# Optimization experiments

Hardware: AMD Instinct MI355X
Metric: run time of the kernel (lower is better)

Reference implementation:

```python
import jax, jax.numpy as jnp
import numpy as np

LN_EPS = 1e-5

def setup_inputs() -> dict:
    key = jax.random.key(0)
    ks = jax.random.split(key, 4)
    B, D, H, K = 8192, 4096, 2048, 512
    return {
        "x": jax.random.normal(ks[0], (B, D), jnp.float32),
        "beta": jax.random.normal(ks[1], (D, K), jnp.float32) * 0.01,
        "compound_mean": jnp.zeros((D,), jnp.float32),
        "W1": jax.random.normal(ks[2], (H, D), jnp.float32) * 0.02,
        "b1": jnp.zeros((H,), jnp.float32),
        "ln_w": jnp.ones((H,), jnp.float32),
        "ln_b": jnp.zeros((H,), jnp.float32),
        "W2": jax.random.normal(ks[3], (K, H), jnp.float32) * 0.02,
        "b2": jnp.zeros((K,), jnp.float32),
    }

def reference(x, beta, compound_mean, W1, b1, ln_w, ln_b, W2, b2):
    # compound path of BiQBMVAE.forward (compound=True)
    h = jnp.einsum('bd,hd->bh', x - compound_mean, W1) + b1      # fc1
    mu = jnp.mean(h, axis=-1, keepdims=True)                      # LayerNorm
    var = jnp.mean(jnp.square(h - mu), axis=-1, keepdims=True)
    h = (h - mu) * jax.lax.rsqrt(var + LN_EPS) * ln_w + ln_b
    h = jax.nn.relu(h)                                            # act_fn
    q_logits = jnp.einsum('bh,kh->bk', h, W2) + b2                # fc2 -> [B, k]
    x_recon = jax.nn.sigmoid(jnp.einsum('bk,dk->bd', q_logits, beta))  # decode_compound
    return (q_logits, x_recon, q_logits, q_logits)
```

## Files before the change

kernel.cpp:

```cpp
#include <hip/hip_runtime.h>
#include <hip/hip_bf16.h>
#include <cstddef>
#include <cstdint>

#define LN_EPS 1e-5f

#define B_DIM 8192
#define D_DIM 4096
#define H_DIM 2048
#define K_DIM 512

typedef __bf16 bf16x8_t __attribute__((ext_vector_type(8)));
typedef float f32x4_t __attribute__((ext_vector_type(4)));

__device__ __forceinline__ void gl2lds16(const __hip_bfloat16* g,
                                         __hip_bfloat16* l) {
  __builtin_amdgcn_global_load_lds(
      (const __attribute__((address_space(1))) uint32_t*)g,
      (__attribute__((address_space(3))) uint32_t*)l, 16, 0, 0);
}

__global__ __launch_bounds__(256) void conv_x_kernel(
    const float* __restrict__ x, const float* __restrict__ cmean,
    __hip_bfloat16* __restrict__ out) {
  const long i = (((long)blockIdx.x << 8) + threadIdx.x) << 3;
  const int col = (int)(i & (D_DIM - 1));
  const float4 a = *(const float4*)(x + i);
  const float4 b = *(const float4*)(x + i + 4);
  const float4 ma = *(const float4*)(cmean + col);
  const float4 mb = *(const float4*)(cmean + col + 4);
  union { __hip_bfloat16 h[8]; uint4 u; } pk;
  pk.h[0] = __float2bfloat16(a.x - ma.x);
  pk.h[1] = __float2bfloat16(a.y - ma.y);
  pk.h[2] = __float2bfloat16(a.z - ma.z);
  pk.h[3] = __float2bfloat16(a.w - ma.w);
  pk.h[4] = __float2bfloat16(b.x - mb.x);
  pk.h[5] = __float2bfloat16(b.y - mb.y);
  pk.h[6] = __float2bfloat16(b.z - mb.z);
  pk.h[7] = __float2bfloat16(b.w - mb.w);
  *(uint4*)(out + i) = pk.u;
}

__global__ __launch_bounds__(256) void conv_w3_kernel(
    const float* __restrict__ W1, const float* __restrict__ W2,
    const float* __restrict__ beta, __hip_bfloat16* __restrict__ W1b,
    __hip_bfloat16* __restrict__ W2b, __hip_bfloat16* __restrict__ betab) {
  const int blk = blockIdx.x;
  const float* src;
  __hip_bfloat16* dst;
  long base;
  if (blk < 4096) {
    src = W1; dst = W1b; base = blk;
  } else if (blk < 4608) {
    src = W2; dst = W2b; base = blk - 4096;
  } else {
    src = beta; dst = betab; base = blk - 4608;
  }
  const long i = ((base << 8) + threadIdx.x) << 3;
  const float4 a = *(const float4*)(src + i);
  const float4 b = *(const float4*)(src + i + 4);
  union { __hip_bfloat16 h[8]; uint4 u; } pk;
  pk.h[0] = __float2bfloat16(a.x);
  pk.h[1] = __float2bfloat16(a.y);
  pk.h[2] = __float2bfloat16(a.z);
  pk.h[3] = __float2bfloat16(a.w);
  pk.h[4] = __float2bfloat16(b.x);
  pk.h[5] = __float2bfloat16(b.y);
  pk.h[6] = __float2bfloat16(b.z);
  pk.h[7] = __float2bfloat16(b.w);
  *(uint4*)(dst + i) = pk.u;
}

template <int EPI>
__global__ __launch_bounds__(256) void gemm_bt(
    const __hip_bfloat16* __restrict__ A, int lda,
    const __hip_bfloat16* __restrict__ Bm, int ldb,
    const float* __restrict__ bias, float* __restrict__ C0, int ldc,
    float* __restrict__ C2, float* __restrict__ C3,
    __hip_bfloat16* __restrict__ Cb, int Kd) {
  __shared__ __hip_bfloat16 lA[128 * 32];
  __shared__ __hip_bfloat16 lB[128 * 32];

  const int t = threadIdx.x;
  const int lane = t & 63;
  const int wv = t >> 6;
  const int wm = (wv >> 1) * 64;
  const int wn = (wv & 1) * 64;
  const int fr = lane & 15;
  const int ko = lane >> 4;
  const int kos = (ko ^ ((fr >> 1) & 3)) * 8;

  const long rowA = (long)blockIdx.y * 128;
  const long rowB = (long)blockIdx.x * 128;

  const int ci = wv * 128 + lane;
  const int srow = ci >> 2;
  const int scol = (((ci & 3) ^ ((ci >> 3) & 3))) * 8;
  const __hip_bfloat16* pA0 = A + (rowA + srow) * (long)lda + scol;
  const __hip_bfloat16* pA1 = pA0 + 16L * lda;
  const __hip_bfloat16* pB0 = Bm + (rowB + srow) * (long)ldb + scol;
  const __hip_bfloat16* pB1 = pB0 + 16L * ldb;
  __hip_bfloat16* lA0 = lA + wv * 128 * 8;
  __hip_bfloat16* lA1 = lA0 + 64 * 8;
  __hip_bfloat16* lB0 = lB + wv * 128 * 8;
  __hip_bfloat16* lB1 = lB0 + 64 * 8;

  f32x4_t acc[4][4];
  const f32x4_t zero = {0.f, 0.f, 0.f, 0.f};
#pragma unroll
  for (int mi = 0; mi < 4; ++mi)
#pragma unroll
    for (int ni = 0; ni < 4; ++ni) acc[mi][ni] = zero;

  for (int k0 = 0; k0 < Kd; k0 += 32) {
    gl2lds16(pA0 + k0, lA0);
    gl2lds16(pA1 + k0, lA1);
    gl2lds16(pB0 + k0, lB0);
    gl2lds16(pB1 + k0, lB1);
    __syncthreads();

    bf16x8_t af[4], bfv[4];
#pragma unroll
    for (int mi = 0; mi < 4; ++mi)
      af[mi] = *(const bf16x8_t*)&lA[(wm + mi * 16 + fr) * 32 + kos];
#pragma unroll
    for (int ni = 0; ni < 4; ++ni)
      bfv[ni] = *(const bf16x8_t*)&lB[(wn + ni * 16 + fr) * 32 + kos];
#pragma unroll
    for (int mi = 0; mi < 4; ++mi)
#pragma unroll
      for (int ni = 0; ni < 4; ++ni)
        acc[mi][ni] = __builtin_amdgcn_mfma_f32_16x16x32_bf16(
            af[mi], bfv[ni], acc[mi][ni], 0, 0, 0);
    __syncthreads();
  }

  const long cRow0 = rowA + wm;
  const int cCol0 = (int)rowB + wn;
#pragma unroll
  for (int mi = 0; mi < 4; ++mi) {
#pragma unroll
    for (int ni = 0; ni < 4; ++ni) {
      f32x4_t a = acc[mi][ni];
      int col = cCol0 + ni * 16 + fr;
#pragma unroll
      for (int r = 0; r < 4; ++r) {
        long row = cRow0 + mi * 16 + ko * 4 + r;
        float val = a[r];
        if constexpr (EPI == 0) {
          val += bias[col];
          C0[row * (long)ldc + col] = val;
        } else if constexpr (EPI == 1) {
          val += bias[col];
          C0[row * (long)ldc + col] = val;
          C2[row * (long)ldc + col] = val;
          C3[row * (long)ldc + col] = val;
          Cb[row * (long)ldc + col] = __float2bfloat16(val);
        } else {
          val = 1.f / (1.f + __expf(-val));
          C0[row * (long)ldc + col] = val;
        }
      }
    }
  }
}

template <int EPI>
__global__ __launch_bounds__(512, 2) void gemm256_bt(
    const __hip_bfloat16* __restrict__ A, int lda,
    const __hip_bfloat16* __restrict__ Bm, int ldb,
    const float* __restrict__ bias, float* __restrict__ C0, int ldc, int Kd) {
  constexpr int SLOT = 16384;
  __shared__ __hip_bfloat16 lds[3 * SLOT];

  const int t_ = threadIdx.x;
  const int lane = t_ & 63;
  const int wv = t_ >> 6;
  const int wr = wv >> 2;
  const int wc = wv & 3;
  const int fr = lane & 15;
  const int ko = lane >> 4;
  const int kos = (ko ^ ((fr >> 1) & 3)) * 8;

  const long rowA = (long)blockIdx.y * 256;
  const long rowB = (long)blockIdx.x * 256;

  const int ci = (wv << 6) + lane;
  const int srow = ci >> 2;
  const int scol = ((ci & 3) ^ ((ci >> 3) & 3)) << 3;
  const __hip_bfloat16* pA0 = A + (rowA + srow) * (long)lda + scol;
  const __hip_bfloat16* pA1 = pA0 + 128L * lda;
  const __hip_bfloat16* pB0 = Bm + (rowB + srow) * (long)ldb + scol;
  const __hip_bfloat16* pB1 = pB0 + 128L * ldb;

  f32x4_t acc[8][4];
  const f32x4_t zero = {0.f, 0.f, 0.f, 0.f};
#pragma unroll
  for (int mi = 0; mi < 8; ++mi)
#pragma unroll
    for (int ni = 0; ni < 4; ++ni) acc[mi][ni] = zero;

  const int NT = Kd >> 5;

  {
    __hip_bfloat16* a0 = lds + wv * 512;
    gl2lds16(pA0, a0);
    gl2lds16(pA1, a0 + 4096);
    __hip_bfloat16* b0 = lds + 8192 + wv * 512;
    gl2lds16(pB0, b0);
    gl2lds16(pB1, b0 + 4096);
  }
  if (NT > 1) {
    __hip_bfloat16* a1 = lds + SLOT + wv * 512;
    gl2lds16(pA0 + 32, a1);
    gl2lds16(pA1 + 32, a1 + 4096);
    __hip_bfloat16* b1 = lds + SLOT + 8192 + wv * 512;
    gl2lds16(pB0 + 32, b1);
    gl2lds16(pB1 + 32, b1 + 4096);
    asm volatile("s_waitcnt vmcnt(4)" ::: "memory");
  } else {
    asm volatile("s_waitcnt vmcnt(0)" ::: "memory");
  }
  __builtin_amdgcn_s_barrier();
  __builtin_amdgcn_sched_barrier(0);

  for (int t = 0; t < NT; ++t) {
    const int slot = t % 3;
    const int nslot = (t + 2) % 3;
    const __hip_bfloat16* sA = lds + slot * SLOT;
    const __hip_bfloat16* sB = sA + 8192;
    const int kk = (t + 2) << 5;
    const bool pf = (t + 2) < NT;

    bf16x8_t af[4], bfv[4];
#pragma unroll
    for (int mi = 0; mi < 4; ++mi)
      af[mi] = *(const bf16x8_t*)&sA[(wr * 128 + mi * 16 + fr) * 32 + kos];
#pragma unroll
    for (int ni = 0; ni < 4; ++ni)
      bfv[ni] = *(const bf16x8_t*)&sB[(wc * 64 + ni * 16 + fr) * 32 + kos];
    if (pf) {
      __hip_bfloat16* la = lds + nslot * SLOT + wv * 512;
      gl2lds16(pA0 + kk, la);
      gl2lds16(pA1 + kk, la + 4096);
    }
    __builtin_amdgcn_s_setprio(1);
#pragma unroll
    for (int mi = 0; mi < 4; ++mi)
#pragma unroll
      for (int ni = 0; ni < 4; ++ni)
        acc[mi][ni] = __builtin_amdgcn_mfma_f32_16x16x32_bf16(
            af[mi], bfv[ni], acc[mi][ni], 0, 0, 0);
    __builtin_amdgcn_s_setprio(0);

    bf16x8_t ag[4];
#pragma unroll
    for (int mi = 0; mi < 4; ++mi)
      ag[mi] =
          *(const bf16x8_t*)&sA[(wr * 128 + 64 + mi * 16 + fr) * 32 + kos];
    if (pf) {
      __hip_bfloat16* lb = lds + nslot * SLOT + 8192 + wv * 512;
      gl2lds16(pB0 + kk, lb);
      gl2lds16(pB1 + kk, lb + 4096);
    }
    __builtin_amdgcn_s_setprio(1);
#pragma unroll
    for (int mi = 0; mi < 4; ++mi)
#pragma unroll
      for (int ni = 0; ni < 4; ++ni)
        acc[4 + mi][ni] = __builtin_amdgcn_mfma_f32_16x16x32_bf16(
            ag[mi], bfv[ni], acc[4 + mi][ni], 0, 0, 0);
    __builtin_amdgcn_s_setprio(0);

    if (t + 1 < NT) {
      if (pf)
        asm volatile("s_waitcnt vmcnt(4)" ::: "memory");
      else
        asm volatile("s_waitcnt vmcnt(0)" ::: "memory");
      __builtin_amdgcn_s_barrier();
      __builtin_amdgcn_sched_barrier(0);
    }
  }

  const long cRow0 = rowA + wr * 128;
  const int cCol0 = (int)rowB + wc * 64;
#pragma unroll
  for (int mi = 0; mi < 8; ++mi) {
#pragma unroll
    for (int ni = 0; ni < 4; ++ni) {
      f32x4_t a = acc[mi][ni];
      const int col = cCol0 + ni * 16 + fr;
#pragma unroll
      for (int r = 0; r < 4; ++r) {
        const long row = cRow0 + mi * 16 + ko * 4 + r;
        float val = a[r];
        if constexpr (EPI == 0) {
          val += bias[col];
        } else {
          val = 1.f / (1.f + __expf(-val));
        }
        C0[row * (long)ldc + col] = val;
      }
    }
  }
}

__global__ __launch_bounds__(256) void ln_relu_kernel(
    void* hptr, const float* __restrict__ ln_w, const float* __restrict__ ln_b) {
  const int H = H_DIM;
  float* h = (float*)hptr;
  __hip_bfloat16* hb = (__hip_bfloat16*)hptr;

  const long row = blockIdx.x;
  const int t = threadIdx.x;
  const int lane = t & 63;
  const int wv = t >> 6;
  const float* hr = h + row * H;

  float v[8];
#pragma unroll
  for (int i = 0; i < 8; ++i) v[i] = hr[t + i * 256];

  __shared__ float red[8];

  float s = 0.f;
#pragma unroll
  for (int i = 0; i < 8; ++i) s += v[i];
#pragma unroll
  for (int off = 32; off; off >>= 1) s += __shfl_down(s, off);
  if (lane == 0) red[wv] = s;
  __syncthreads();
  const float mu = (red[0] + red[1] + red[2] + red[3]) * (1.f / (float)H);

  float vs = 0.f;
#pragma unroll
  for (int i = 0; i < 8; ++i) {
    float d = v[i] - mu;
    vs += d * d;
  }
#pragma unroll
  for (int off = 32; off; off >>= 1) vs += __shfl_down(vs, off);
  if (lane == 0) red[4 + wv] = vs;
  __syncthreads();
  const float var = (red[4] + red[5] + red[6] + red[7]) * (1.f / (float)H);
  const float rs = rsqrtf(var + LN_EPS);

  __hip_bfloat16* hbr = hb + row * (long)D_DIM;
#pragma unroll
  for (int i = 0; i < 8; ++i) {
    int col = t + i * 256;
    float y = (v[i] - mu) * rs * ln_w[col] + ln_b[col];
    y = fmaxf(y, 0.f);
    hbr[col] = __float2bfloat16(y);
  }
}

extern "C" void kernel_launch(void* const* d_in, const int* in_sizes, int n_in,
                              void* d_out, int out_size, void* d_ws,
                              size_t ws_size, hipStream_t stream) {
  const float* x = (const float*)d_in[0];
  const float* beta = (const float*)d_in[1];
  const float* cmean = (const float*)d_in[2];
  const float* W1 = (const float*)d_in[3];
  const float* b1 = (const float*)d_in[4];
  const float* ln_w = (const float*)d_in[5];
  const float* ln_b = (const float*)d_in[6];
  const float* W2 = (const float*)d_in[7];
  const float* b2 = (const float*)d_in[8];

  float* out = (float*)d_out;
  float* q0 = out;
  float* xr = out + (size_t)B_DIM * K_DIM;
  float* q2 = xr + (size_t)B_DIM * D_DIM;
  float* q3 = q2 + (size_t)B_DIM * K_DIM;

  __hip_bfloat16* xb = (__hip_bfloat16*)xr;
  float* h = xr + (size_t)B_DIM * D_DIM / 2;
  __hip_bfloat16* hb = (__hip_bfloat16*)h;

  __hip_bfloat16* W1b = (__hip_bfloat16*)d_ws;
  __hip_bfloat16* W2b = W1b + (size_t)H_DIM * D_DIM;
  __hip_bfloat16* betab = W2b + (size_t)K_DIM * H_DIM;
  __hip_bfloat16* qb = betab + (size_t)D_DIM * K_DIM;

  dim3 blk(256, 1, 1);
  dim3 blk512(512, 1, 1);

  hipLaunchKernelGGL(conv_x_kernel, dim3((B_DIM * (size_t)D_DIM) / 2048), blk,
                     0, stream, x, cmean, xb);
  hipLaunchKernelGGL(conv_w3_kernel, dim3(4096 + 512 + 1024), blk, 0, stream,
                     W1, W2, beta, W1b, W2b, betab);

  hipLaunchKernelGGL((gemm256_bt<0>), dim3(H_DIM / 256, B_DIM / 256), blk512,
                     0, stream, xb, D_DIM, W1b, D_DIM, b1, h, H_DIM, D_DIM);

  hipLaunchKernelGGL(ln_relu_kernel, dim3(B_DIM), blk, 0, stream, (void*)h,
                     ln_w, ln_b);

  hipLaunchKernelGGL((gemm_bt<1>), dim3(K_DIM / 128, B_DIM / 128), blk, 0,
                     stream, hb, D_DIM, W2b, H_DIM, b2, q0, K_DIM, q2, q3, qb,
                     H_DIM);

  hipLaunchKernelGGL((gemm256_bt<2>), dim3(D_DIM / 256, B_DIM / 256), blk512,
                     0, stream, qb, K_DIM, betab, K_DIM, (const float*)nullptr,
                     xr, D_DIM, K_DIM);
}
```

Measured before the change: 546.2 us.

## Use 4-slot LDS ring with register prefetch and swizzled block order for GEMMs

Replaces the GEMM kernels with ring-buffered variants. Global-to-LDS prefetch now runs three tiles ahead across four slots, and the next tile's fragments are double-buffered in registers, so each k-step needs a single barrier. Workgroups are remapped in an XCD-aware interleaved order to improve L2 locality. The fc2 GEMM moves to a 512-thread, 4-wave-per-SIMD pipelined 128x128 kernel, and the decode GEMM switches from 256x256 to 128x128 tiles. The cost is more LDS per block and register pressure from the duplicated fragment buffers.

```diff
diff --git a/kernel.cpp b/kernel.cpp
--- a/kernel.cpp
+++ b/kernel.cpp
@@ -72,85 +72,262 @@
 }
 
 template <int EPI>
-__global__ __launch_bounds__(256) void gemm_bt(
+__global__ __launch_bounds__(512, 2) void gemm256_ring(
+    const __hip_bfloat16* __restrict__ A, int lda,
+    const __hip_bfloat16* __restrict__ Bm, int ldb,
+    const float* __restrict__ bias, float* __restrict__ C0, int ldc, int Kd) {
+  constexpr int SLOT = 16384;
+  __shared__ __hip_bfloat16 lds[4 * SLOT];
+
+  const int t_ = threadIdx.x;
+  const int lane = t_ & 63;
+  const int wv = t_ >> 6;
+  const int wr = wv >> 2;
+  const int wc = wv & 3;
+  const int fr = lane & 15;
+  const int ko = lane >> 4;
+  const int kos = (ko ^ ((fr >> 1) & 3)) * 8;
+
+  const int gx = gridDim.x;
+  const int nwg = gx * gridDim.y;
+  const int f = blockIdx.y * gx + blockIdx.x;
+  const int w = (f & 7) * (nwg >> 3) + (f >> 3);
+  const int bx = w % gx;
+  const int by = w / gx;
+
+  const long rowA = (long)by * 256;
+  const long rowB = (long)bx * 256;
+
+  const int ci = (wv << 6) + lane;
+  const int srow = ci >> 2;
+  const int skq = (ci & 3) ^ ((ci >> 3) & 3);
+  const __hip_bfloat16* sA0 = A + (rowA + srow) * (long)lda + skq * 8;
+  const __hip_bfloat16* sA1 = sA0 + 128L * lda;
+  const __hip_bfloat16* sB0 = Bm + (rowB + srow) * (long)ldb + skq * 8;
+  const __hip_bfloat16* sB1 = sB0 + 128L * ldb;
+
+  auto STG = [&](int s, int k0) {
+    __hip_bfloat16* d = lds + s * SLOT + wv * 512;
+    gl2lds16(sA0 + k0, d);
+    gl2lds16(sA1 + k0, d + 4096);
+    gl2lds16(sB0 + k0, d + 8192);
+    gl2lds16(sB1 + k0, d + 12288);
+  };
+
+  f32x4_t acc[8][4];
+  const f32x4_t zero = {0.f, 0.f, 0.f, 0.f};
+#pragma unroll
+  for (int a = 0; a < 8; ++a)
+#pragma unroll
+    for (int b = 0; b < 4; ++b) acc[a][b] = zero;
+
+  const int NT = Kd >> 5;
+
+  STG(0, 0);
+  STG(1, 32);
+  STG(2, 64);
+  asm volatile("s_waitcnt vmcnt(4)" ::: "memory");
+  __builtin_amdgcn_s_barrier();
+  __builtin_amdgcn_sched_barrier(0);
+
+  bf16x8_t F0a[4], F0b[4], F1a[4], F1b[4];
+#pragma unroll
+  for (int mi = 0; mi < 4; ++mi)
+    F0a[mi] = *(const bf16x8_t*)&lds[(wr * 128 + mi * 16 + fr) * 32 + kos];
+#pragma unroll
+  for (int ni = 0; ni < 4; ++ni)
+    F0b[ni] =
+        *(const bf16x8_t*)&lds[8192 + (wc * 64 + ni * 16 + fr) * 32 + kos];
+
+  auto BODY = [&](int t, bf16x8_t(&cf)[4], bf16x8_t(&cb)[4],
+                  bf16x8_t(&nf)[4], bf16x8_t(&nb)[4]) {
+    const int st = (t & 3) * SLOT;
+    if (t + 3 < NT) STG((t + 3) & 3, (t + 3) * 32);
+    bf16x8_t ag[4];
+#pragma unroll
+    for (int mi = 0; mi < 4; ++mi)
+      ag[mi] =
+          *(const bf16x8_t*)&lds[st + (wr * 128 + 64 + mi * 16 + fr) * 32 +
+                                 kos];
+    if (t + 1 < NT) {
+      const int s1 = ((t + 1) & 3) * SLOT;
+#pragma unroll
+      for (int mi = 0; mi < 4; ++mi)
+        nf[mi] =
+            *(const bf16x8_t*)&lds[s1 + (wr * 128 + mi * 16 + fr) * 32 + kos];
+#pragma unroll
+      for (int ni = 0; ni < 4; ++ni)
+        nb[ni] = *(const bf16x8_t*)&lds[s1 + 8192 +
+                                        (wc * 64 + ni * 16 + fr) * 32 + kos];
+    }
+    __builtin_amdgcn_s_setprio(1);
+#pragma unroll
+    for (int mi = 0; mi < 4; ++mi)
+#pragma unroll
+      for (int ni = 0; ni < 4; ++ni)
+        acc[mi][ni] = __builtin_amdgcn_mfma_f32_16x16x32_bf16(
+            cf[mi], cb[ni], acc[mi][ni], 0, 0, 0);
+#pragma unroll
+    for (int mi = 0; mi < 4; ++mi)
+#pragma unroll
+      for (int ni = 0; ni < 4; ++ni)
+        acc[4 + mi][ni] = __builtin_amdgcn_mfma_f32_16x16x32_bf16(
+            ag[mi], cb[ni], acc[4 + mi][ni], 0, 0, 0);
+    __builtin_amdgcn_s_setprio(0);
+    if (t + 1 < NT) {
+      if (t + 3 < NT)
+        asm volatile("s_waitcnt vmcnt(4)" ::: "memory");
+      else
+        asm volatile("s_waitcnt vmcnt(0)" ::: "memory");
+      __builtin_amdgcn_s_barrier();
+      __builtin_amdgcn_sched_barrier(0);
+    }
+  };
+
+  for (int t = 0; t < NT; t += 2) {
+    BODY(t, F0a, F0b, F1a, F1b);
+    BODY(t + 1, F1a, F1b, F0a, F0b);
+  }
+
+  const long cRow0 = rowA + wr * 128;
+  const int cCol0 = (int)rowB + wc * 64;
+#pragma unroll
+  for (int a = 0; a < 8; ++a) {
+#pragma unroll
+    for (int b = 0; b < 4; ++b) {
+      f32x4_t v4 = acc[a][b];
+      const int col = cCol0 + b * 16 + fr;
+#pragma unroll
+      for (int r = 0; r < 4; ++r) {
+        const long row = cRow0 + a * 16 + ko * 4 + r;
+        float val = v4[r];
+        if constexpr (EPI == 0) {
+          val += bias[col];
+        } else {
+          val = 1.f / (1.f + __expf(-val));
+        }
+        C0[row * (long)ldc + col] = val;
+      }
+    }
+  }
+}
+
+template <int EPI>
+__global__ __launch_bounds__(512, 4) void gemm128_ring(
     const __hip_bfloat16* __restrict__ A, int lda,
     const __hip_bfloat16* __restrict__ Bm, int ldb,
     const float* __restrict__ bias, float* __restrict__ C0, int ldc,
     float* __restrict__ C2, float* __restrict__ C3,
     __hip_bfloat16* __restrict__ Cb, int Kd) {
-  __shared__ __hip_bfloat16 lA[128 * 32];
-  __shared__ __hip_bfloat16 lB[128 * 32];
-
-  const int t = threadIdx.x;
-  const int lane = t & 63;
-  const int wv = t >> 6;
-  const int wm = (wv >> 1) * 64;
-  const int wn = (wv & 1) * 64;
+  constexpr int SLOT = 8192;
+  __shared__ __hip_bfloat16 lds[4 * SLOT];
+
+  const int t_ = threadIdx.x;
+  const int lane = t_ & 63;
+  const int wv = t_ >> 6;
+  const int wr = wv >> 2;
+  const int wc = wv & 3;
   const int fr = lane & 15;
   const int ko = lane >> 4;
   const int kos = (ko ^ ((fr >> 1) & 3)) * 8;
 
-  const long rowA = (long)blockIdx.y * 128;
-  const long rowB = (long)blockIdx.x * 128;
-
-  const int ci = wv * 128 + lane;
+  const int gx = gridDim.x;
+  const int nwg = gx * gridDim.y;
+  const int f = blockIdx.y * gx + blockIdx.x;
+  const int w = (f & 7) * (nwg >> 3) + (f >> 3);
+  const int bx = w % gx;
+  const int by = w / gx;
+
+  const long rowA = (long)by * 128;
+  const long rowB = (long)bx * 128;
+
+  const int ci = (wv << 6) + lane;
   const int srow = ci >> 2;
-  const int scol = (((ci & 3) ^ ((ci >> 3) & 3))) * 8;
-  const __hip_bfloat16* pA0 = A + (rowA + srow) * (long)lda + scol;
-  const __hip_bfloat16* pA1 = pA0 + 16L * lda;
-  const __hip_bfloat16* pB0 = Bm + (rowB + srow) * (long)ldb + scol;
-  const __hip_bfloat16* pB1 = pB0 + 16L * ldb;
-  __hip_bfloat16* lA0 = lA + wv * 128 * 8;
-  __hip_bfloat16* lA1 = lA0 + 64 * 8;
-  __hip_bfloat16* lB0 = lB + wv * 128 * 8;
-  __hip_bfloat16* lB1 = lB0 + 64 * 8;
-
-  f32x4_t acc[4][4];
+  const int skq = (ci & 3) ^ ((ci >> 3) & 3);
+  const __hip_bfloat16* sA = A + (rowA + srow) * (long)lda + skq * 8;
+  const __hip_bfloat16* sB = Bm + (rowB + srow) * (long)ldb + skq * 8;
+
+  auto STG = [&](int s, int k0) {
+    __hip_bfloat16* d = lds + s * SLOT + wv * 512;
+    gl2lds16(sA + k0, d);
+    gl2lds16(sB + k0, d + 4096);
+  };
+
+  f32x4_t acc[4][2];
   const f32x4_t zero = {0.f, 0.f, 0.f, 0.f};
 #pragma unroll
+  for (int a = 0; a < 4; ++a)
+#pragma unroll
+    for (int b = 0; b < 2; ++b) acc[a][b] = zero;
+
+  const int NT = Kd >> 5;
+
+  STG(0, 0);
+  STG(1, 32);
+  STG(2, 64);
+  asm volatile("s_waitcnt vmcnt(2)" ::: "memory");
+  __builtin_amdgcn_s_barrier();
+  __builtin_amdgcn_sched_barrier(0);
+
+  bf16x8_t F0a[4], F0b[2], F1a[4], F1b[2];
+#pragma unroll
   for (int mi = 0; mi < 4; ++mi)
-#pragma unroll
-    for (int ni = 0; ni < 4; ++ni) acc[mi][ni] = zero;
-
-  for (int k0 = 0; k0 < Kd; k0 += 32) {
-    gl2lds16(pA0 + k0, lA0);
-    gl2lds16(pA1 + k0, lA1);
-    gl2lds16(pB0 + k0, lB0);
-    gl2lds16(pB1 + k0, lB1);
-    __syncthreads();
-
-    bf16x8_t af[4], bfv[4];
+    F0a[mi] = *(const bf16x8_t*)&lds[(wr * 64 + mi * 16 + fr) * 32 + kos];
+#pragma unroll
+  for (int ni = 0; ni < 2; ++ni)
+    F0b[ni] =
+        *(const bf16x8_t*)&lds[4096 + (wc * 32 + ni * 16 + fr) * 32 + kos];
+
+  auto BODY = [&](int t, bf16x8_t(&cf)[4], bf16x8_t(&cb)[2],
+                  bf16x8_t(&nf)[4], bf16x8_t(&nb)[2]) {
+    if (t + 3 < NT) STG((t + 3) & 3, (t + 3) * 32);
+    if (t + 1 < NT) {
+      const int s1 = ((t + 1) & 3) * SLOT;
+#pragma unroll
+      for (int mi = 0; mi < 4; ++mi)
+        nf[mi] =
+            *(const bf16x8_t*)&lds[s1 + (wr * 64 + mi * 16 + fr) * 32 + kos];
+#pragma unroll
+      for (int ni = 0; ni < 2; ++ni)
+        nb[ni] = *(const bf16x8_t*)&lds[s1 + 4096 +
+                                        (wc * 32 + ni * 16 + fr) * 32 + kos];
+    }
+    __builtin_amdgcn_s_setprio(1);
 #pragma unroll
     for (int mi = 0; mi < 4; ++mi)
-      af[mi] = *(const bf16x8_t*)&lA[(wm + mi * 16 + fr) * 32 + kos];
-#pragma unroll
-    for (int ni = 0; ni < 4; ++ni)
-      bfv[ni] = *(const bf16x8_t*)&lB[(wn + ni * 16 + fr) * 32 + kos];
-#pragma unroll
-    for (int mi = 0; mi < 4; ++mi)
-#pragma unroll
-      for (int ni = 0; ni < 4; ++ni)
+#pragma unroll
+      for (int ni = 0; ni < 2; ++ni)
         acc[mi][ni] = __builtin_amdgcn_mfma_f32_16x16x32_bf16(
-            af[mi], bfv[ni], acc[mi][ni], 0, 0, 0);
-    __syncthreads();
-  }
-
-  const long cRow0 = rowA + wm;
-  const int cCol0 = (int)rowB + wn;
-#pragma unroll
-  for (int mi = 0; mi < 4; ++mi) {
-#pragma unroll
-    for (int ni = 0; ni < 4; ++ni) {
-      f32x4_t a = acc[mi][ni];
-      int col = cCol0 + ni * 16 + fr;
+            cf[mi], cb[ni], acc[mi][ni], 0, 0, 0);
+    __builtin_amdgcn_s_setprio(0);
+    if (t + 1 < NT) {
+      if (t + 3 < NT)
+        asm volatile("s_waitcnt vmcnt(2)" ::: "memory");
+      else
+        asm volatile("s_waitcnt vmcnt(0)" ::: "memory");
+      __builtin_amdgcn_s_barrier();
+      __builtin_amdgcn_sched_barrier(0);
+    }
+  };
+
+  for (int t = 0; t < NT; t += 2) {
+    BODY(t, F0a, F0b, F1a, F1b);
+    BODY(t + 1, F1a, F1b, F0a, F0b);
+  }
+
+  const long cRow0 = rowA + wr * 64;
+  const int cCol0 = (int)rowB + wc * 32;
+#pragma unroll
+  for (int a = 0; a < 4; ++a) {
+#pragma unroll
+    for (int b = 0; b < 2; ++b) {
+      f32x4_t v4 = acc[a][b];
+      const int col = cCol0 + b * 16 + fr;
 #pragma unroll
       for (int r = 0; r < 4; ++r) {
-        long row = cRow0 + mi * 16 + ko * 4 + r;
-        float val = a[r];
-        if constexpr (EPI == 0) {
-          val += bias[col];
-          C0[row * (long)ldc + col] = val;
-        } else if constexpr (EPI == 1) {
+        const long row = cRow0 + a * 16 + ko * 4 + r;
+        float val = v4[r];
+        if constexpr (EPI == 1) {
           val += bias[col];
           C0[row * (long)ldc + col] = val;
           C2[row * (long)ldc + col] = val;
@@ -160,146 +337,6 @@
           val = 1.f / (1.f + __expf(-val));
           C0[row * (long)ldc + col] = val;
         }
-      }
-    }
-  }
-}
-
-template <int EPI>
-__global__ __launch_bounds__(512, 2) void gemm256_bt(
-    const __hip_bfloat16* __restrict__ A, int lda,
-    const __hip_bfloat16* __restrict__ Bm, int ldb,
-    const float* __restrict__ bias, float* __restrict__ C0, int ldc, int Kd) {
-  constexpr int SLOT = 16384;
-  __shared__ __hip_bfloat16 lds[3 * SLOT];
-
-  const int t_ = threadIdx.x;
-  const int lane = t_ & 63;
-  const int wv = t_ >> 6;
-  const int wr = wv >> 2;
-  const int wc = wv & 3;
-  const int fr = lane & 15;
-  const int ko = lane >> 4;
-  const int kos = (ko ^ ((fr >> 1) & 3)) * 8;
-
-  const long rowA = (long)blockIdx.y * 256;
-  const long rowB = (long)blockIdx.x * 256;
-
-  const int ci = (wv << 6) + lane;
-  const int srow = ci >> 2;
-  const int scol = ((ci & 3) ^ ((ci >> 3) & 3)) << 3;
-  const __hip_bfloat16* pA0 = A + (rowA + srow) * (long)lda + scol;
-  const __hip_bfloat16* pA1 = pA0 + 128L * lda;
-  const __hip_bfloat16* pB0 = Bm + (rowB + srow) * (long)ldb + scol;
-  const __hip_bfloat16* pB1 = pB0 + 128L * ldb;
-
-  f32x4_t acc[8][4];
-  const f32x4_t zero = {0.f, 0.f, 0.f, 0.f};
-#pragma unroll
-  for (int mi = 0; mi < 8; ++mi)
-#pragma unroll
-    for (int ni = 0; ni < 4; ++ni) acc[mi][ni] = zero;
-
-  const int NT = Kd >> 5;
-
-  {
-    __hip_bfloat16* a0 = lds + wv * 512;
-    gl2lds16(pA0, a0);
-    gl2lds16(pA1, a0 + 4096);
-    __hip_bfloat16* b0 = lds + 8192 + wv * 512;
-    gl2lds16(pB0, b0);
-    gl2lds16(pB1, b0 + 4096);
-  }
-  if (NT > 1) {
-    __hip_bfloat16* a1 = lds + SLOT + wv * 512;
-    gl2lds16(pA0 + 32, a1);
-    gl2lds16(pA1 + 32, a1 + 4096);
-    __hip_bfloat16* b1 = lds + SLOT + 8192 + wv * 512;
-    gl2lds16(pB0 + 32, b1);
-    gl2lds16(pB1 + 32, b1 + 4096);
-    asm volatile("s_waitcnt vmcnt(4)" ::: "memory");
-  } else {
-    asm volatile("s_waitcnt vmcnt(0)" ::: "memory");
-  }
-  __builtin_amdgcn_s_barrier();
-  __builtin_amdgcn_sched_barrier(0);
-
-  for (int t = 0; t < NT; ++t) {
-    const int slot = t % 3;
-    const int nslot = (t + 2) % 3;
-    const __hip_bfloat16* sA = lds + slot * SLOT;
-    const __hip_bfloat16* sB = sA + 8192;
-    const int kk = (t + 2) << 5;
-    const bool pf = (t + 2) < NT;
-
-    bf16x8_t af[4], bfv[4];
-#pragma unroll
-    for (int mi = 0; mi < 4; ++mi)
-      af[mi] = *(const bf16x8_t*)&sA[(wr * 128 + mi * 16 + fr) * 32 + kos];
-#pragma unroll
-    for (int ni = 0; ni < 4; ++ni)
-      bfv[ni] = *(const bf16x8_t*)&sB[(wc * 64 + ni * 16 + fr) * 32 + kos];
-    if (pf) {
-      __hip_bfloat16* la = lds + nslot * SLOT + wv * 512;
-      gl2lds16(pA0 + kk, la);
-      gl2lds16(pA1 + kk, la + 4096);
-    }
-    __builtin_amdgcn_s_setprio(1);
-#pragma unroll
-    for (int mi = 0; mi < 4; ++mi)
-#pragma unroll
-      for (int ni = 0; ni < 4; ++ni)
-        acc[mi][ni] = __builtin_amdgcn_mfma_f32_16x16x32_bf16(
-            af[mi], bfv[ni], acc[mi][ni], 0, 0, 0);
-    __builtin_amdgcn_s_setprio(0);
-
-    bf16x8_t ag[4];
-#pragma unroll
-    for (int mi = 0; mi < 4; ++mi)
-      ag[mi] =
-          *(const bf16x8_t*)&sA[(wr * 128 + 64 + mi * 16 + fr) * 32 + kos];
-    if (pf) {
-      __hip_bfloat16* lb = lds + nslot * SLOT + 8192 + wv * 512;
-      gl2lds16(pB0 + kk, lb);
-      gl2lds16(pB1 + kk, lb + 4096);
-    }
-    __builtin_amdgcn_s_setprio(1);
-#pragma unroll
-    for (int mi = 0; mi < 4; ++mi)
-#pragma unroll
-      for (int ni = 0; ni < 4; ++ni)
-        acc[4 + mi][ni] = __builtin_amdgcn_mfma_f32_16x16x32_bf16(
-            ag[mi], bfv[ni], acc[4 + mi][ni], 0, 0, 0);
-    __builtin_amdgcn_s_setprio(0);
-
-    if (t + 1 < NT) {
-      if (pf)
-        asm volatile("s_waitcnt vmcnt(4)" ::: "memory");
-      else
-        asm volatile("s_waitcnt vmcnt(0)" ::: "memory");
-      __builtin_amdgcn_s_barrier();
-      __builtin_amdgcn_sched_barrier(0);
-    }
-  }
-
-  const long cRow0 = rowA + wr * 128;
-  const int cCol0 = (int)rowB + wc * 64;
-#pragma unroll
-  for (int mi = 0; mi < 8; ++mi) {
-#pragma unroll
-    for (int ni = 0; ni < 4; ++ni) {
-      f32x4_t a = acc[mi][ni];
-      const int col = cCol0 + ni * 16 + fr;
-#pragma unroll
-      for (int r = 0; r < 4; ++r) {
-        const long row = cRow0 + mi * 16 + ko * 4 + r;
-        float val = a[r];
-        if constexpr (EPI == 0) {
-          val += bias[col];
-        } else {
-          val = 1.f / (1.f + __expf(-val));
-        }
-        C0[row * (long)ldc + col] = val;
       }
     }
   }
@@ -391,17 +428,19 @@
   hipLaunchKernelGGL(conv_w3_kernel, dim3(4096 + 512 + 1024), blk, 0, stream,
                      W1, W2, beta, W1b, W2b, betab);
 
-  hipLaunchKernelGGL((gemm256_bt<0>), dim3(H_DIM / 256, B_DIM / 256), blk512,
-                     0, stream, xb, D_DIM, W1b, D_DIM, b1, h, H_DIM, D_DIM);
+  hipLaunchKernelGGL((gemm256_ring<0>), dim3(H_DIM / 256, B_DIM / 256),
+                     blk512, 0, stream, xb, D_DIM, W1b, D_DIM, b1, h, H_DIM,
+                     D_DIM);
 
   hipLaunchKernelGGL(ln_relu_kernel, dim3(B_DIM), blk, 0, stream, (void*)h,
                      ln_w, ln_b);
 
-  hipLaunchKernelGGL((gemm_bt<1>), dim3(K_DIM / 128, B_DIM / 128), blk, 0,
-                     stream, hb, D_DIM, W2b, H_DIM, b2, q0, K_DIM, q2, q3, qb,
-                     H_DIM);
-
-  hipLaunchKernelGGL((gemm256_bt<2>), dim3(D_DIM / 256, B_DIM / 256), blk512,
-                     0, stream, qb, K_DIM, betab, K_DIM, (const float*)nullptr,
-                     xr, D_DIM, K_DIM);
-}
+  hipLaunchKernelGGL((gemm128_ring<1>), dim3(K_DIM / 128, B_DIM / 128),
+                     blk512, 0, stream, hb, D_DIM, W2b, H_DIM, b2, q0, K_DIM,
+                     q2, q3, qb, H_DIM);
+
+  hipLaunchKernelGGL((gemm128_ring<2>), dim3(D_DIM / 128, B_DIM / 128),
+                     blk512, 0, stream, qb, K_DIM, betab, K_DIM,
+                     (const float*)nullptr, xr, D_DIM, (float*)nullptr,
+                     (float*)nullptr, (__hip_bfloat16*)nullptr, K_DIM);
+}
```

New measurement: 534.1 us. -2.2%, faster.
